# Kernel optimization log

Hardware: AMD Instinct MI355X
Metric: run time of the kernel (lower is better)

## Reference

```python
import jax, jax.numpy as jnp
import numpy as np

EPS = 1e-5

def _bn(x, gamma, beta):
    # BatchNorm with track_running_stats=False: batch stats over all dims but last
    axes = tuple(range(x.ndim - 1))
    mu = jnp.mean(x, axis=axes)
    var = jnp.var(x, axis=axes)  # biased, as torch uses for normalization
    return (x - mu) * jax.lax.rsqrt(var + EPS) * gamma + beta

def setup_inputs() -> dict:
    B, N, D = 8, 200, 128
    key = jax.random.key(0)
    ks = jax.random.split(key, 14)
    s = 1.0 / np.sqrt(D)
    def w(k):
        return jax.random.uniform(k, (D, D), jnp.float32, -s, s)
    def b(k):
        return jax.random.uniform(k, (D,), jnp.float32, -s, s)
    return {
        'h': jax.random.normal(ks[0], (B, N, D), jnp.float32),
        'e': jax.random.normal(ks[1], (B, N, N, D), jnp.float32),
        'Uw': w(ks[2]), 'Ub': b(ks[3]),
        'Vw': w(ks[4]), 'Vb': b(ks[5]),
        'Aw': w(ks[6]), 'Ab': b(ks[7]),
        'Bw': w(ks[8]), 'Bb': b(ks[9]),
        'Cw': w(ks[10]), 'Cb': b(ks[11]),
        'gamma_h': jnp.ones((D,), jnp.float32), 'beta_h': jnp.zeros((D,), jnp.float32),
        'gamma_e': jnp.ones((D,), jnp.float32), 'beta_e': jnp.zeros((D,), jnp.float32),
    }

def reference(h, e, Uw, Ub, Vw, Vb, Aw, Ab, Bw, Bb, Cw, Cb,
              gamma_h, beta_h, gamma_e, beta_e):
    h_in, e_in = h, e
    Uh = h @ Uw.T + Ub                      # [B,N,D]
    Vh = h @ Vw.T + Vb                      # [B,N,D]
    Ah = h @ Aw.T + Ab
    Bh = h @ Bw.T + Bb
    Ce = e @ Cw.T + Cb                      # [B,N,N,D]
    # e_new[b,i,j,d] = Ah[b,j,d] + Bh[b,i,d] + Ce[b,i,j,d]
    e_new = Ah[:, None, :, :] + Bh[:, :, None, :] + Ce
    gates = jax.nn.sigmoid(e_new)           # [B,N,N,D]
    # sum aggregation over source nodes j with Vh broadcast over i
    agg = jnp.sum(gates * Vh[:, None, :, :], axis=2)  # [B,N,D]
    h_new = Uh + agg
    h_out = h_in + jax.nn.relu(_bn(h_new, gamma_h, beta_h))
    e_out = e_in + jax.nn.relu(_bn(e_new, gamma_e, beta_e))
    return (h_out, e_out)
```

## Files before the change

kernel.cpp:

```cpp
#include <hip/hip_runtime.h>


#define B_ 8
#define N_ 200
#define D_ 128
#define BN_ (B_*N_)
#define HN_ (BN_*D_)

typedef __attribute__((ext_vector_type(8))) short short8v;
typedef __attribute__((ext_vector_type(4))) short short4v;
typedef __attribute__((ext_vector_type(4))) float float4v;
typedef __attribute__((ext_vector_type(4))) unsigned int uint4v;

__device__ __forceinline__ unsigned short f2b(float f) {
  unsigned u = __float_as_uint(f);
  u += 0x7FFFu + ((u >> 16) & 1u);
  return (unsigned short)(u >> 16);
}

__device__ __forceinline__ short8v cvt_bf16x8(float4v lo, float4v hi) {
  unsigned int r0, r1, r2, r3;
  asm("v_cvt_pk_bf16_f32 %0, %1, %2" : "=v"(r0) : "v"(lo.x), "v"(lo.y));
  asm("v_cvt_pk_bf16_f32 %0, %1, %2" : "=v"(r1) : "v"(lo.z), "v"(lo.w));
  asm("v_cvt_pk_bf16_f32 %0, %1, %2" : "=v"(r2) : "v"(hi.x), "v"(hi.y));
  asm("v_cvt_pk_bf16_f32 %0, %1, %2" : "=v"(r3) : "v"(hi.z), "v"(hi.w));
  uint4v u; u.x = r0; u.y = r1; u.z = r2; u.w = r3;
  return __builtin_bit_cast(short8v, u);
}

__global__ __launch_bounds__(256) void prelin_kernel(
    const float* __restrict__ h,
    const float* __restrict__ Uw, const float* __restrict__ Ub,
    const float* __restrict__ Vw, const float* __restrict__ Vb,
    const float* __restrict__ Aw, const float* __restrict__ Ab,
    const float* __restrict__ Bw, const float* __restrict__ Bb,
    const float* __restrict__ Cw, const float* __restrict__ Cb,
    float* __restrict__ Uh, float* __restrict__ VhT,
    float* __restrict__ Ah, float* __restrict__ AhT,
    float* __restrict__ BhC,
    unsigned short* __restrict__ Cwbf) {
  const int tid = threadIdx.x;
  if (blockIdx.x >= 100) {
    int g = (blockIdx.x - 100) * 1024 + tid * 4;
    float4v v = *(const float4v*)(Cw + g);
    short4v s;
    s.x = (short)f2b(v.x); s.y = (short)f2b(v.y);
    s.z = (short)f2b(v.z); s.w = (short)f2b(v.w);
    *(short4v*)(Cwbf + g) = s;
    return;
  }
  const int r0 = blockIdx.x * 16;
  __shared__ float hs[16][128];
  for (int k = 0; k < 2; k++) {
    int g = k * 256 + tid;
    int row = g >> 5, col4 = g & 31;
    *(float4v*)&hs[row][col4 * 4] =
        *(const float4v*)(h + (size_t)(r0 + row) * D_ + col4 * 4);
  }
  __syncthreads();
  const int c0 = tid, c1 = tid + 256;
  const float* w0 = (c0 < 128) ? (Uw + c0 * 128) : (Vw + (c0 - 128) * 128);
  const float  b0 = (c0 < 128) ? Ub[c0] : Vb[c0 - 128];
  const float* w1 = (c1 < 384) ? (Aw + (c1 - 256) * 128) : (Bw + (c1 - 384) * 128);
  const float  b1 = (c1 < 384) ? Ab[c1 - 256] : (Bb[c1 - 384] + Cb[c1 - 384]);
  float acc0[16], acc1[16];
#pragma unroll
  for (int r = 0; r < 16; r++) { acc0[r] = 0.f; acc1[r] = 0.f; }
  for (int k = 0; k < 128; k += 4) {
    float4v w0v = *(const float4v*)(w0 + k);
    float4v w1v = *(const float4v*)(w1 + k);
#pragma unroll
    for (int r = 0; r < 16; r++) {
      float4v hv = *(const float4v*)&hs[r][k];
      acc0[r] = fmaf(hv.x, w0v.x, fmaf(hv.y, w0v.y, fmaf(hv.z, w0v.z, fmaf(hv.w, w0v.w, acc0[r]))));
      acc1[r] = fmaf(hv.x, w1v.x, fmaf(hv.y, w1v.y, fmaf(hv.z, w1v.z, fmaf(hv.w, w1v.w, acc1[r]))));
    }
  }
  const int cc0 = c0 & 127;
  const int cc1 = (c1 - 256) & 127;
#pragma unroll
  for (int r = 0; r < 16; r++) {
    const int g = r0 + r;
    const int bb = g / 200;
    const int ii = g - bb * 200;
    float v0 = acc0[r] + b0;
    if (c0 < 128) Uh[(size_t)g * D_ + cc0] = v0;
    else          VhT[((size_t)bb * D_ + cc0) * N_ + ii] = v0;
    float v1 = acc1[r] + b1;
    if (c1 < 384) {
      Ah[(size_t)g * D_ + cc1] = v1;
      AhT[((size_t)bb * D_ + cc1) * N_ + ii] = v1;
    } else {
      BhC[(size_t)g * D_ + cc1] = v1;
    }
  }
}

template <int MODE>
__global__ __launch_bounds__(256, 2) void gemm_pass(
    const float* __restrict__ e, const unsigned short* __restrict__ Cwbf,
    const float* __restrict__ BhC, const float* __restrict__ Ah,
    const float* __restrict__ AhT, const float* __restrict__ VhT,
    float* __restrict__ agg, float* __restrict__ psum, float* __restrict__ psumsq,
    const float* __restrict__ scale_e, const float* __restrict__ shift_e,
    float* __restrict__ e_out,
    const float* __restrict__ hin, const float* __restrict__ Uh,
    const float* __restrict__ scale_h, const float* __restrict__ shift_h,
    float* __restrict__ h_out) {
  const int tid = threadIdx.x;

  if (MODE == 1 && blockIdx.x >= BN_) {
    const int idx = (blockIdx.x - BN_) * 256 + tid;
    float4v u = ((const float4v*)Uh)[idx];
    float4v a = ((const float4v*)agg)[idx];
    float4v hv = ((const float4v*)hin)[idx];
    float4v sc = ((const float4v*)scale_h)[idx & 31];
    float4v sh = ((const float4v*)shift_h)[idx & 31];
    float4v o;
#pragma unroll
    for (int l = 0; l < 4; l++) {
      float y = fmaxf(fmaf(u[l] + a[l], sc[l], sh[l]), 0.f);
      o[l] = hv[l] + y;
    }
    ((float4v*)h_out)[idx] = o;
    return;
  }

  const int blk = blockIdx.x;
  const int b = blk / N_;
  const int lane = tid & 63, wz = tid >> 6;
  const int c = lane & 15, q = lane >> 4;

  __shared__ __align__(16) unsigned short Bs[128 * 128];

  const uint4v* bsrc = (const uint4v*)Cwbf;
#pragma unroll
  for (int k2 = 0; k2 < 8; k2++) {
    int g = k2 * 256 + tid;
    int row = g >> 4;
    int col16 = (g & 15) ^ (row & 7);
    *(uint4v*)&Bs[row * 128 + col16 * 8] = bsrc[g];
  }

  float bsev[8];
  if (MODE == 0) {
#pragma unroll
    for (int t = 0; t < 8; t++) bsev[t] = BhC[(size_t)blk * D_ + t * 16 + c];
  }
  __syncthreads();

  const float* erow = e + (size_t)blk * N_ * D_;
  const float* AhB = Ah + (size_t)b * N_ * D_;
  const float* AhTb = AhT + (size_t)b * D_ * N_;
  const float* VhTb = VhT + (size_t)b * D_ * N_;
  const float* BhCrow = BhC + (size_t)blk * D_;

  float aggv[8], sumv[8], sqv[8];
  if (MODE == 0) {
#pragma unroll
    for (int t = 0; t < 8; t++) { aggv[t] = 0.f; sumv[t] = 0.f; sqv[t] = 0.f; }
  }

  const int sw = c & 7;

  float4v ef[8];
  {
    const int j = wz * 16 + c;
    const float* p = erow + (size_t)j * D_ + q * 8;
    const bool ok = (j < N_);
#pragma unroll
    for (int l = 0; l < 4; l++) {
      ef[2 * l]     = ok ? *(const float4v*)(p + l * 32)     : (float4v){0.f,0.f,0.f,0.f};
      ef[2 * l + 1] = ok ? *(const float4v*)(p + l * 32 + 4) : (float4v){0.f,0.f,0.f,0.f};
    }
  }

#pragma unroll
  for (int jt = 0; jt < 4; jt++) {
    const int j0 = jt * 64;
    short8v av[4];
#pragma unroll
    for (int l = 0; l < 4; l++) av[l] = cvt_bf16x8(ef[2 * l], ef[2 * l + 1]);

    if (jt < 3) {
      const int j = (jt + 1) * 64 + wz * 16 + c;
      const float* p = erow + (size_t)j * D_ + q * 8;
      const bool ok = (j < N_);
#pragma unroll
      for (int l = 0; l < 4; l++) {
        ef[2 * l]     = ok ? *(const float4v*)(p + l * 32)     : (float4v){0.f,0.f,0.f,0.f};
        ef[2 * l + 1] = ok ? *(const float4v*)(p + l * 32 + 4) : (float4v){0.f,0.f,0.f,0.f};
      }
    }

    float4v acc[8];
#pragma unroll
    for (int t = 0; t < 8; t++) acc[t] = (float4v){0.f, 0.f, 0.f, 0.f};
#pragma unroll
    for (int t = 0; t < 8; t++) {
      const unsigned short* brow = &Bs[(t * 16 + c) * 128];
#pragma unroll
      for (int l = 0; l < 4; l++) {
        short8v cw = *(const short8v*)(brow + (((q | (l << 2)) ^ sw) << 3));
        if (MODE == 0)
          acc[t] = __builtin_amdgcn_mfma_f32_16x16x32_bf16(av[l], cw, acc[t], 0, 0, 0);
        else
          acc[t] = __builtin_amdgcn_mfma_f32_16x16x32_bf16(cw, av[l], acc[t], 0, 0, 0);
      }
    }

    if (MODE == 0) {
      const int jb = j0 + wz * 16 + q * 4;
      if (jb < N_) {
        const float* pA = AhTb + (size_t)c * N_ + jb;
        const float* pV = VhTb + (size_t)c * N_ + jb;
#pragma unroll
        for (int t = 0; t < 8; t++) {
          float4v ah4 = *(const float4v*)(pA + (size_t)t * 16 * N_);
          float4v vh4 = *(const float4v*)(pV + (size_t)t * 16 * N_);
          const float bse = bsev[t];
          float ag = aggv[t], sm = sumv[t], sq2 = sqv[t];
#pragma unroll
          for (int r = 0; r < 4; r++) {
            float x = acc[t][r] + bse + ah4[r];
            float g = __builtin_amdgcn_rcpf(1.0f + __expf(-x));
            ag = fmaf(g, vh4[r], ag);
            sm += x;
            sq2 = fmaf(x, x, sq2);
          }
          aggv[t] = ag; sumv[t] = sm; sqv[t] = sq2;
        }
      }
    } else {
      const int j = j0 + wz * 16 + c;
      if (j < N_) {
        const size_t rowoff = (size_t)blk * N_ * D_ + (size_t)j * D_;
#pragma unroll
        for (int t = 0; t < 8; t++) {
          const int n4 = t * 16 + q * 4;
          float4v ah = *(const float4v*)(AhB + (size_t)j * D_ + n4);
          float4v bs4 = *(const float4v*)(BhCrow + n4);
          float4v sc4 = *(const float4v*)(scale_e + n4);
          float4v sh4 = *(const float4v*)(shift_e + n4);
          float4v ein = *(const float4v*)(e + rowoff + n4);
          float4v o;
#pragma unroll
          for (int r = 0; r < 4; r++) {
            float x = acc[t][r] + bs4[r] + ah[r];
            float y = fmaxf(fmaf(x, sc4[r], sh4[r]), 0.f);
            o[r] = ein[r] + y;
          }
          *(float4v*)(e_out + rowoff + n4) = o;
        }
      }
    }
  }

  if (MODE == 0) {
    __syncthreads();
    float* red = (float*)Bs;
#pragma unroll
    for (int t = 0; t < 8; t++) {
      float a = aggv[t], s = sumv[t], sq2 = sqv[t];
      a += __shfl_xor(a, 16); a += __shfl_xor(a, 32);
      s += __shfl_xor(s, 16); s += __shfl_xor(s, 32);
      sq2 += __shfl_xor(sq2, 16); sq2 += __shfl_xor(sq2, 32);
      if (q == 0) {
        red[(0 * 4 + wz) * 128 + t * 16 + c] = a;
        red[(1 * 4 + wz) * 128 + t * 16 + c] = s;
        red[(2 * 4 + wz) * 128 + t * 16 + c] = sq2;
      }
    }
    __syncthreads();
    if (tid < 128) {
      float a = 0.f, s = 0.f, sq2 = 0.f;
#pragma unroll
      for (int w = 0; w < 4; w++) {
        a += red[(0 * 4 + w) * 128 + tid];
        s += red[(1 * 4 + w) * 128 + tid];
        sq2 += red[(2 * 4 + w) * 128 + tid];
      }
      agg[(size_t)blk * D_ + tid] = a;
      psum[(size_t)blk * D_ + tid] = s;
      psumsq[(size_t)blk * D_ + tid] = sq2;
    }
  }
}

__global__ __launch_bounds__(256) void stats_part(
    const float* __restrict__ psum, const float* __restrict__ psumsq,
    const float* __restrict__ Uh, const float* __restrict__ agg,
    float* __restrict__ partial) {
  const int t = threadIdx.x, blk = blockIdx.x;
  const int cg = t & 31, rs = t >> 5;
  float4v ps = {0,0,0,0}, pq = {0,0,0,0}, hs = {0,0,0,0}, hq = {0,0,0,0};
#pragma unroll
  for (int p = 0; p < 2; p++) {
    const int row = blk * 16 + p * 8 + rs;
    const size_t off = (size_t)row * D_ + cg * 4;
    float4v a = *(const float4v*)(psum + off);
    float4v bq = *(const float4v*)(psumsq + off);
    float4v u = *(const float4v*)(Uh + off);
    float4v g = *(const float4v*)(agg + off);
    ps += a; pq += bq;
    float4v hv = u + g;
    hs += hv; hq += hv * hv;
  }
  __shared__ float4v red[4][8][32];
  red[0][rs][cg] = ps; red[1][rs][cg] = pq; red[2][rs][cg] = hs; red[3][rs][cg] = hq;
  __syncthreads();
  if (t < 128) {
    const int s = t >> 5, g = t & 31;
    float4v acc = red[s][0][g];
#pragma unroll
    for (int r = 1; r < 8; r++) acc += red[s][r][g];
    *(float4v*)(partial + (size_t)blk * 512 + s * 128 + g * 4) = acc;
  }
}

__global__ __launch_bounds__(256) void stats_final(
    const float* __restrict__ partial,
    const float* __restrict__ gamma_h, const float* __restrict__ beta_h,
    const float* __restrict__ gamma_e, const float* __restrict__ beta_e,
    float* __restrict__ scale_e, float* __restrict__ shift_e,
    float* __restrict__ scale_h, float* __restrict__ shift_h) {
  const int t = threadIdx.x;
  const int n = t & 127;
  if (t < 128) {
    float s = 0.f, sq = 0.f;
    for (int p = 0; p < 100; p++) {
      const float* base = partial + (size_t)p * 512;
      s += base[n]; sq += base[128 + n];
    }
    const float Me = 8.f * 200.f * 200.f;
    float mean = s / Me;
    float var = sq / Me - mean * mean;
    float sce = gamma_e[n] * rsqrtf(var + 1e-5f);
    scale_e[n] = sce; shift_e[n] = beta_e[n] - mean * sce;
  } else {
    float hs = 0.f, hq = 0.f;
    for (int p = 0; p < 100; p++) {
      const float* base = partial + (size_t)p * 512;
      hs += base[256 + n]; hq += base[384 + n];
    }
    const float Mh = (float)BN_;
    float mh = hs / Mh;
    float vh = hq / Mh - mh * mh;
    float sch = gamma_h[n] * rsqrtf(vh + 1e-5f);
    scale_h[n] = sch; shift_h[n] = beta_h[n] - mh * sch;
  }
}

extern "C" void kernel_launch(void* const* d_in, const int* in_sizes, int n_in,
                              void* d_out, int out_size, void* d_ws, size_t ws_size,
                              hipStream_t stream) {
  const float* h  = (const float*)d_in[0];
  const float* e  = (const float*)d_in[1];
  const float* Uw = (const float*)d_in[2];  const float* Ub = (const float*)d_in[3];
  const float* Vw = (const float*)d_in[4];  const float* Vb = (const float*)d_in[5];
  const float* Aw = (const float*)d_in[6];  const float* Ab = (const float*)d_in[7];
  const float* Bw = (const float*)d_in[8];  const float* Bb = (const float*)d_in[9];
  const float* Cw = (const float*)d_in[10]; const float* Cb = (const float*)d_in[11];
  const float* gamma_h = (const float*)d_in[12]; const float* beta_h = (const float*)d_in[13];
  const float* gamma_e = (const float*)d_in[14]; const float* beta_e = (const float*)d_in[15];

  float* ws = (float*)d_ws;
  float* Uh   = ws + 0;
  float* VhT  = ws + (size_t)HN_;
  float* Ah   = ws + (size_t)HN_ * 2;
  float* BhC  = ws + (size_t)HN_ * 3;
  float* agg  = ws + (size_t)HN_ * 4;
  float* psum = ws + (size_t)HN_ * 5;
  float* psumsq = ws + (size_t)HN_ * 6;
  float* AhT  = ws + (size_t)HN_ * 7;
  float* scale_e = ws + (size_t)HN_ * 8;
  float* shift_e = scale_e + 128;
  float* scale_h = scale_e + 256;
  float* shift_h = scale_e + 384;
  unsigned short* Cwbf = (unsigned short*)(scale_e + 512);
  float* partial = scale_e + 512 + 8192;

  float* h_out = (float*)d_out;
  float* e_out = (float*)d_out + HN_;

  prelin_kernel<<<116, 256, 0, stream>>>(h, Uw, Ub, Vw, Vb, Aw, Ab, Bw, Bb, Cw, Cb,
                                         Uh, VhT, Ah, AhT, BhC, Cwbf);
  gemm_pass<0><<<BN_, 256, 0, stream>>>(e, Cwbf, BhC, Ah, AhT, VhT,
                                        agg, psum, psumsq,
                                        nullptr, nullptr, nullptr,
                                        nullptr, nullptr, nullptr, nullptr, nullptr);
  stats_part<<<100, 256, 0, stream>>>(psum, psumsq, Uh, agg, partial);
  stats_final<<<1, 256, 0, stream>>>(partial, gamma_h, beta_h, gamma_e, beta_e,
                                     scale_e, shift_e, scale_h, shift_h);
  gemm_pass<1><<<BN_ + 200, 256, 0, stream>>>(e, Cwbf, BhC, Ah, AhT, VhT,
                                              agg, psum, psumsq,
                                              scale_e, shift_e, e_out,
                                              h, Uh, scale_h, shift_h, h_out);
}
```

Measured before the change: 462.5 us.

## Interleave per-tile MFMA with epilogue and raise occupancy to four blocks

```diff
diff --git a/kernel.cpp b/kernel.cpp
--- a/kernel.cpp
+++ b/kernel.cpp
@@ -97,7 +97,7 @@
 }
 
 template <int MODE>
-__global__ __launch_bounds__(256, 2) void gemm_pass(
+__global__ __launch_bounds__(256, 4) void gemm_pass(
     const float* __restrict__ e, const unsigned short* __restrict__ Cwbf,
     const float* __restrict__ BhC, const float* __restrict__ Ah,
     const float* __restrict__ AhT, const float* __restrict__ VhT,
@@ -141,12 +141,6 @@
     int col16 = (g & 15) ^ (row & 7);
     *(uint4v*)&Bs[row * 128 + col16 * 8] = bsrc[g];
   }
-
-  float bsev[8];
-  if (MODE == 0) {
-#pragma unroll
-    for (int t = 0; t < 8; t++) bsev[t] = BhC[(size_t)blk * D_ + t * 16 + c];
-  }
   __syncthreads();
 
   const float* erow = e + (size_t)blk * N_ * D_;
@@ -154,6 +148,7 @@
   const float* AhTb = AhT + (size_t)b * D_ * N_;
   const float* VhTb = VhT + (size_t)b * D_ * N_;
   const float* BhCrow = BhC + (size_t)blk * D_;
+  const float* BhCc = BhCrow + c;
 
   float aggv[8], sumv[8], sqv[8];
   if (MODE == 0) {
@@ -193,36 +188,37 @@
       }
     }
 
-    float4v acc[8];
-#pragma unroll
-    for (int t = 0; t < 8; t++) acc[t] = (float4v){0.f, 0.f, 0.f, 0.f};
+    const int jb = j0 + wz * 16 + q * 4;
+    const bool ok0 = (jb < N_);
+    const float* pA = AhTb + (size_t)c * N_ + jb;
+    const float* pV = VhTb + (size_t)c * N_ + jb;
+    const int j1 = j0 + wz * 16 + c;
+    const bool ok1 = (j1 < N_);
+    const size_t rowoff = (size_t)blk * (N_ * D_) + (size_t)j1 * D_;
+    const float* pAh1 = AhB + (size_t)j1 * D_ + q * 4;
+
 #pragma unroll
     for (int t = 0; t < 8; t++) {
+      float4v acc = (float4v){0.f, 0.f, 0.f, 0.f};
       const unsigned short* brow = &Bs[(t * 16 + c) * 128];
 #pragma unroll
       for (int l = 0; l < 4; l++) {
         short8v cw = *(const short8v*)(brow + (((q | (l << 2)) ^ sw) << 3));
         if (MODE == 0)
-          acc[t] = __builtin_amdgcn_mfma_f32_16x16x32_bf16(av[l], cw, acc[t], 0, 0, 0);
+          acc = __builtin_amdgcn_mfma_f32_16x16x32_bf16(av[l], cw, acc, 0, 0, 0);
         else
-          acc[t] = __builtin_amdgcn_mfma_f32_16x16x32_bf16(cw, av[l], acc[t], 0, 0, 0);
-      }
-    }
-
-    if (MODE == 0) {
-      const int jb = j0 + wz * 16 + q * 4;
-      if (jb < N_) {
-        const float* pA = AhTb + (size_t)c * N_ + jb;
-        const float* pV = VhTb + (size_t)c * N_ + jb;
-#pragma unroll
-        for (int t = 0; t < 8; t++) {
-          float4v ah4 = *(const float4v*)(pA + (size_t)t * 16 * N_);
-          float4v vh4 = *(const float4v*)(pV + (size_t)t * 16 * N_);
-          const float bse = bsev[t];
+          acc = __builtin_amdgcn_mfma_f32_16x16x32_bf16(cw, av[l], acc, 0, 0, 0);
+      }
+
+      if (MODE == 0) {
+        if (ok0) {
+          float4v ah4 = *(const float4v*)(pA + (size_t)t * (16 * N_));
+          float4v vh4 = *(const float4v*)(pV + (size_t)t * (16 * N_));
+          const float bse = BhCc[t * 16];
           float ag = aggv[t], sm = sumv[t], sq2 = sqv[t];
 #pragma unroll
           for (int r = 0; r < 4; r++) {
-            float x = acc[t][r] + bse + ah4[r];
+            float x = acc[r] + bse + ah4[r];
             float g = __builtin_amdgcn_rcpf(1.0f + __expf(-x));
             ag = fmaf(g, vh4[r], ag);
             sm += x;
@@ -230,15 +226,10 @@
           }
           aggv[t] = ag; sumv[t] = sm; sqv[t] = sq2;
         }
-      }
-    } else {
-      const int j = j0 + wz * 16 + c;
-      if (j < N_) {
-        const size_t rowoff = (size_t)blk * N_ * D_ + (size_t)j * D_;
-#pragma unroll
-        for (int t = 0; t < 8; t++) {
+      } else {
+        if (ok1) {
           const int n4 = t * 16 + q * 4;
-          float4v ah = *(const float4v*)(AhB + (size_t)j * D_ + n4);
+          float4v ah = *(const float4v*)(pAh1 + t * 16);
           float4v bs4 = *(const float4v*)(BhCrow + n4);
           float4v sc4 = *(const float4v*)(scale_e + n4);
           float4v sh4 = *(const float4v*)(shift_e + n4);
@@ -246,7 +237,7 @@
           float4v o;
 #pragma unroll
           for (int r = 0; r < 4; r++) {
-            float x = acc[t][r] + bs4[r] + ah[r];
+            float x = acc[r] + bs4[r] + ah[r];
             float y = fmaxf(fmaf(x, sc4[r], sh4[r]), 0.f);
             o[r] = ein[r] + y;
           }
```

Measured after the change: 688.2 us. 48.8% more time.

## Store pre-norm edge values once and replace second GEMM pass with elementwise epilogue

Applied to the files above, without the earlier changes.

```diff
diff --git a/kernel.cpp b/kernel.cpp
--- a/kernel.cpp
+++ b/kernel.cpp
@@ -36,8 +36,7 @@
     const float* __restrict__ Bw, const float* __restrict__ Bb,
     const float* __restrict__ Cw, const float* __restrict__ Cb,
     float* __restrict__ Uh, float* __restrict__ VhT,
-    float* __restrict__ Ah, float* __restrict__ AhT,
-    float* __restrict__ BhC,
+    float* __restrict__ AhT, float* __restrict__ BhC,
     unsigned short* __restrict__ Cwbf) {
   const int tid = threadIdx.x;
   if (blockIdx.x >= 100) {
@@ -88,7 +87,6 @@
     else          VhT[((size_t)bb * D_ + cc0) * N_ + ii] = v0;
     float v1 = acc1[r] + b1;
     if (c1 < 384) {
-      Ah[(size_t)g * D_ + cc1] = v1;
       AhT[((size_t)bb * D_ + cc1) * N_ + ii] = v1;
     } else {
       BhC[(size_t)g * D_ + cc1] = v1;
@@ -96,36 +94,13 @@
   }
 }
 
-template <int MODE>
-__global__ __launch_bounds__(256, 2) void gemm_pass(
+__global__ __launch_bounds__(256, 2) void gemm_x(
     const float* __restrict__ e, const unsigned short* __restrict__ Cwbf,
-    const float* __restrict__ BhC, const float* __restrict__ Ah,
-    const float* __restrict__ AhT, const float* __restrict__ VhT,
+    const float* __restrict__ BhC, const float* __restrict__ AhT,
+    const float* __restrict__ VhT,
     float* __restrict__ agg, float* __restrict__ psum, float* __restrict__ psumsq,
-    const float* __restrict__ scale_e, const float* __restrict__ shift_e,
-    float* __restrict__ e_out,
-    const float* __restrict__ hin, const float* __restrict__ Uh,
-    const float* __restrict__ scale_h, const float* __restrict__ shift_h,
-    float* __restrict__ h_out) {
+    float* __restrict__ xout) {
   const int tid = threadIdx.x;
-
-  if (MODE == 1 && blockIdx.x >= BN_) {
-    const int idx = (blockIdx.x - BN_) * 256 + tid;
-    float4v u = ((const float4v*)Uh)[idx];
-    float4v a = ((const float4v*)agg)[idx];
-    float4v hv = ((const float4v*)hin)[idx];
-    float4v sc = ((const float4v*)scale_h)[idx & 31];
-    float4v sh = ((const float4v*)shift_h)[idx & 31];
-    float4v o;
-#pragma unroll
-    for (int l = 0; l < 4; l++) {
-      float y = fmaxf(fmaf(u[l] + a[l], sc[l], sh[l]), 0.f);
-      o[l] = hv[l] + y;
-    }
-    ((float4v*)h_out)[idx] = o;
-    return;
-  }
-
   const int blk = blockIdx.x;
   const int b = blk / N_;
   const int lane = tid & 63, wz = tid >> 6;
@@ -143,23 +118,17 @@
   }
 
   float bsev[8];
-  if (MODE == 0) {
-#pragma unroll
-    for (int t = 0; t < 8; t++) bsev[t] = BhC[(size_t)blk * D_ + t * 16 + c];
-  }
+#pragma unroll
+  for (int t = 0; t < 8; t++) bsev[t] = BhC[(size_t)blk * D_ + t * 16 + c];
   __syncthreads();
 
   const float* erow = e + (size_t)blk * N_ * D_;
-  const float* AhB = Ah + (size_t)b * N_ * D_;
   const float* AhTb = AhT + (size_t)b * D_ * N_;
   const float* VhTb = VhT + (size_t)b * D_ * N_;
-  const float* BhCrow = BhC + (size_t)blk * D_;
 
   float aggv[8], sumv[8], sqv[8];
-  if (MODE == 0) {
-#pragma unroll
-    for (int t = 0; t < 8; t++) { aggv[t] = 0.f; sumv[t] = 0.f; sqv[t] = 0.f; }
-  }
+#pragma unroll
+  for (int t = 0; t < 8; t++) { aggv[t] = 0.f; sumv[t] = 0.f; sqv[t] = 0.f; }
 
   const int sw = c & 7;
 
@@ -202,88 +171,61 @@
 #pragma unroll
       for (int l = 0; l < 4; l++) {
         short8v cw = *(const short8v*)(brow + (((q | (l << 2)) ^ sw) << 3));
-        if (MODE == 0)
-          acc[t] = __builtin_amdgcn_mfma_f32_16x16x32_bf16(av[l], cw, acc[t], 0, 0, 0);
-        else
-          acc[t] = __builtin_amdgcn_mfma_f32_16x16x32_bf16(cw, av[l], acc[t], 0, 0, 0);
+        acc[t] = __builtin_amdgcn_mfma_f32_16x16x32_bf16(av[l], cw, acc[t], 0, 0, 0);
       }
     }
 
-    if (MODE == 0) {
-      const int jb = j0 + wz * 16 + q * 4;
-      if (jb < N_) {
-        const float* pA = AhTb + (size_t)c * N_ + jb;
-        const float* pV = VhTb + (size_t)c * N_ + jb;
-#pragma unroll
-        for (int t = 0; t < 8; t++) {
-          float4v ah4 = *(const float4v*)(pA + (size_t)t * 16 * N_);
-          float4v vh4 = *(const float4v*)(pV + (size_t)t * 16 * N_);
-          const float bse = bsev[t];
-          float ag = aggv[t], sm = sumv[t], sq2 = sqv[t];
-#pragma unroll
-          for (int r = 0; r < 4; r++) {
-            float x = acc[t][r] + bse + ah4[r];
-            float g = __builtin_amdgcn_rcpf(1.0f + __expf(-x));
-            ag = fmaf(g, vh4[r], ag);
-            sm += x;
-            sq2 = fmaf(x, x, sq2);
-          }
-          aggv[t] = ag; sumv[t] = sm; sqv[t] = sq2;
+    const int jb = j0 + wz * 16 + q * 4;
+    if (jb < N_) {
+      const float* pA = AhTb + (size_t)c * N_ + jb;
+      const float* pV = VhTb + (size_t)c * N_ + jb;
+      float* px = xout + (size_t)blk * (N_ * D_) + (size_t)jb * D_ + c;
+#pragma unroll
+      for (int t = 0; t < 8; t++) {
+        float4v ah4 = *(const float4v*)(pA + (size_t)t * (16 * N_));
+        float4v vh4 = *(const float4v*)(pV + (size_t)t * (16 * N_));
+        const float bse = bsev[t];
+        float ag = aggv[t], sm = sumv[t], sq2 = sqv[t];
+#pragma unroll
+        for (int r = 0; r < 4; r++) {
+          float x = acc[t][r] + bse + ah4[r];
+          px[t * 16 + r * D_] = x;
+          float g = __builtin_amdgcn_rcpf(1.0f + __expf(-x));
+          ag = fmaf(g, vh4[r], ag);
+          sm += x;
+          sq2 = fmaf(x, x, sq2);
         }
+        aggv[t] = ag; sumv[t] = sm; sqv[t] = sq2;
       }
-    } else {
-      const int j = j0 + wz * 16 + c;
-      if (j < N_) {
-        const size_t rowoff = (size_t)blk * N_ * D_ + (size_t)j * D_;
-#pragma unroll
-        for (int t = 0; t < 8; t++) {
-          const int n4 = t * 16 + q * 4;
-          float4v ah = *(const float4v*)(AhB + (size_t)j * D_ + n4);
-          float4v bs4 = *(const float4v*)(BhCrow + n4);
-          float4v sc4 = *(const float4v*)(scale_e + n4);
-          float4v sh4 = *(const float4v*)(shift_e + n4);
-          float4v ein = *(const float4v*)(e + rowoff + n4);
-          float4v o;
-#pragma unroll
-          for (int r = 0; r < 4; r++) {
-            float x = acc[t][r] + bs4[r] + ah[r];
-            float y = fmaxf(fmaf(x, sc4[r], sh4[r]), 0.f);
-            o[r] = ein[r] + y;
-          }
-          *(float4v*)(e_out + rowoff + n4) = o;
-        }
-      }
-    }
-  }
-
-  if (MODE == 0) {
-    __syncthreads();
-    float* red = (float*)Bs;
-#pragma unroll
-    for (int t = 0; t < 8; t++) {
-      float a = aggv[t], s = sumv[t], sq2 = sqv[t];
-      a += __shfl_xor(a, 16); a += __shfl_xor(a, 32);
-      s += __shfl_xor(s, 16); s += __shfl_xor(s, 32);
-      sq2 += __shfl_xor(sq2, 16); sq2 += __shfl_xor(sq2, 32);
-      if (q == 0) {
-        red[(0 * 4 + wz) * 128 + t * 16 + c] = a;
-        red[(1 * 4 + wz) * 128 + t * 16 + c] = s;
-        red[(2 * 4 + wz) * 128 + t * 16 + c] = sq2;
-      }
-    }
-    __syncthreads();
-    if (tid < 128) {
-      float a = 0.f, s = 0.f, sq2 = 0.f;
-#pragma unroll
-      for (int w = 0; w < 4; w++) {
-        a += red[(0 * 4 + w) * 128 + tid];
-        s += red[(1 * 4 + w) * 128 + tid];
-        sq2 += red[(2 * 4 + w) * 128 + tid];
-      }
-      agg[(size_t)blk * D_ + tid] = a;
-      psum[(size_t)blk * D_ + tid] = s;
-      psumsq[(size_t)blk * D_ + tid] = sq2;
-    }
+    }
+  }
+
+  __syncthreads();
+  float* red = (float*)Bs;
+#pragma unroll
+  for (int t = 0; t < 8; t++) {
+    float a = aggv[t], s = sumv[t], sq2 = sqv[t];
+    a += __shfl_xor(a, 16); a += __shfl_xor(a, 32);
+    s += __shfl_xor(s, 16); s += __shfl_xor(s, 32);
+    sq2 += __shfl_xor(sq2, 16); sq2 += __shfl_xor(sq2, 32);
+    if (q == 0) {
+      red[(0 * 4 + wz) * 128 + t * 16 + c] = a;
+      red[(1 * 4 + wz) * 128 + t * 16 + c] = s;
+      red[(2 * 4 + wz) * 128 + t * 16 + c] = sq2;
+    }
+  }
+  __syncthreads();
+  if (tid < 128) {
+    float a = 0.f, s = 0.f, sq2 = 0.f;
+#pragma unroll
+    for (int w = 0; w < 4; w++) {
+      a += red[(0 * 4 + w) * 128 + tid];
+      s += red[(1 * 4 + w) * 128 + tid];
+      sq2 += red[(2 * 4 + w) * 128 + tid];
+    }
+    agg[(size_t)blk * D_ + tid] = a;
+    psum[(size_t)blk * D_ + tid] = s;
+    psumsq[(size_t)blk * D_ + tid] = sq2;
   }
 }
 
@@ -351,6 +293,55 @@
   }
 }
 
+__global__ __launch_bounds__(256) void fuse_out(
+    const float* __restrict__ e,
+    const float* __restrict__ scale_e, const float* __restrict__ shift_e,
+    const float* __restrict__ hin, const float* __restrict__ Uh,
+    const float* __restrict__ agg,
+    const float* __restrict__ scale_h, const float* __restrict__ shift_h,
+    float* __restrict__ h_out, float* __restrict__ e_out) {
+  const int tid = threadIdx.x;
+  const int blk = blockIdx.x;
+  if (blk < 200) {
+    const int idx = blk * 256 + tid;
+    float4v u = ((const float4v*)Uh)[idx];
+    float4v a = ((const float4v*)agg)[idx];
+    float4v hv = ((const float4v*)hin)[idx];
+    float4v sc = ((const float4v*)scale_h)[idx & 31];
+    float4v sh = ((const float4v*)shift_h)[idx & 31];
+    float4v o;
+#pragma unroll
+    for (int l = 0; l < 4; l++) {
+      float y = fmaxf(fmaf(u[l] + a[l], sc[l], sh[l]), 0.f);
+      o[l] = hv[l] + y;
+    }
+    ((float4v*)h_out)[idx] = o;
+    return;
+  }
+  const size_t total8 = (size_t)BN_ * N_ * D_ / 8;
+  const size_t stride = (size_t)2048 * 256;
+  for (size_t i = (size_t)(blk - 200) * 256 + tid; i < total8; i += stride) {
+    const size_t base = i * 8;
+    const int n0 = (int)(base & 127);
+    float4v x0 = *(const float4v*)(e_out + base);
+    float4v x1 = *(const float4v*)(e_out + base + 4);
+    float4v e0 = *(const float4v*)(e + base);
+    float4v e1 = *(const float4v*)(e + base + 4);
+    float4v sc0 = *(const float4v*)(scale_e + n0);
+    float4v sc1 = *(const float4v*)(scale_e + n0 + 4);
+    float4v sh0 = *(const float4v*)(shift_e + n0);
+    float4v sh1 = *(const float4v*)(shift_e + n0 + 4);
+    float4v o0, o1;
+#pragma unroll
+    for (int l = 0; l < 4; l++) {
+      o0[l] = e0[l] + fmaxf(fmaf(x0[l], sc0[l], sh0[l]), 0.f);
+      o1[l] = e1[l] + fmaxf(fmaf(x1[l], sc1[l], sh1[l]), 0.f);
+    }
+    *(float4v*)(e_out + base) = o0;
+    *(float4v*)(e_out + base + 4) = o1;
+  }
+}
+
 extern "C" void kernel_launch(void* const* d_in, const int* in_sizes, int n_in,
                               void* d_out, int out_size, void* d_ws, size_t ws_size,
                               hipStream_t stream) {
@@ -367,13 +358,12 @@
   float* ws = (float*)d_ws;
   float* Uh   = ws + 0;
   float* VhT  = ws + (size_t)HN_;
-  float* Ah   = ws + (size_t)HN_ * 2;
+  float* AhT  = ws + (size_t)HN_ * 2;
   float* BhC  = ws + (size_t)HN_ * 3;
   float* agg  = ws + (size_t)HN_ * 4;
   float* psum = ws + (size_t)HN_ * 5;
   float* psumsq = ws + (size_t)HN_ * 6;
-  float* AhT  = ws + (size_t)HN_ * 7;
-  float* scale_e = ws + (size_t)HN_ * 8;
+  float* scale_e = ws + (size_t)HN_ * 7;
   float* shift_e = scale_e + 128;
   float* scale_h = scale_e + 256;
   float* shift_h = scale_e + 384;
@@ -384,16 +374,12 @@
   float* e_out = (float*)d_out + HN_;
 
   prelin_kernel<<<116, 256, 0, stream>>>(h, Uw, Ub, Vw, Vb, Aw, Ab, Bw, Bb, Cw, Cb,
-                                         Uh, VhT, Ah, AhT, BhC, Cwbf);
-  gemm_pass<0><<<BN_, 256, 0, stream>>>(e, Cwbf, BhC, Ah, AhT, VhT,
-                                        agg, psum, psumsq,
-                                        nullptr, nullptr, nullptr,
-                                        nullptr, nullptr, nullptr, nullptr, nullptr);
+                                         Uh, VhT, AhT, BhC, Cwbf);
+  gemm_x<<<BN_, 256, 0, stream>>>(e, Cwbf, BhC, AhT, VhT,
+                                  agg, psum, psumsq, e_out);
   stats_part<<<100, 256, 0, stream>>>(psum, psumsq, Uh, agg, partial);
   stats_final<<<1, 256, 0, stream>>>(partial, gamma_h, beta_h, gamma_e, beta_e,
                                      scale_e, shift_e, scale_h, shift_h);
-  gemm_pass<1><<<BN_ + 200, 256, 0, stream>>>(e, Cwbf, BhC, Ah, AhT, VhT,
-                                              agg, psum, psumsq,
-                                              scale_e, shift_e, e_out,
-                                              h, Uh, scale_h, shift_h, h_out);
-}
+  fuse_out<<<2248, 256, 0, stream>>>(e, scale_e, shift_e, h, Uh, agg,
+                                     scale_h, shift_h, h_out, e_out);
+}
```

Result: slower. 474.1 us (+2.5%).
